# Kernel tuning notes

Hardware: AMD Instinct MI355X
Metric: run time of the kernel (lower is better)

The kernel has to match this reference:

```python
import jax, jax.numpy as jnp
import numpy as np


def gcn_conv(x, src, dst, W, b, n_nodes):
    # PyG GCNConv default: add self-loops, symmetric normalization D^-1/2 A D^-1/2.
    h = x @ W  # [N, out]
    # degree with unit edge weights + self loop
    deg = jnp.zeros((n_nodes,), dtype=x.dtype).at[dst].add(1.0) + 1.0
    dinv = jax.lax.rsqrt(deg)  # deg >= 1, safe
    norm = dinv[src] * dinv[dst]  # [E]
    msg = h[src] * norm[:, None]  # [E, out] gather + scale
    out = jnp.zeros_like(h).at[dst].add(msg)  # scatter-add aggregate
    # self-loop contribution: norm_ii = dinv_i^2
    out = out + h * (dinv * dinv)[:, None]
    return out + b


def setup_inputs() -> dict:
    key = jax.random.key(0)
    ks = jax.random.split(key, 10)
    N, E, F_in, H, G = 100000, 1600000, 128, 128, 256
    x = jax.random.normal(ks[0], (N, F_in), dtype=jnp.float32)
    edge_index = jax.random.randint(ks[1], (2, E), 0, N, dtype=jnp.int64)
    batch = jnp.sort(jax.random.randint(ks[2], (N,), 0, G, dtype=jnp.int64))
    s1 = 1.0 / np.sqrt(F_in)
    s2 = 1.0 / np.sqrt(H)
    W1 = jax.random.uniform(ks[3], (F_in, H), jnp.float32, -s1, s1)
    b1 = jnp.zeros((H,), jnp.float32)
    W2 = jax.random.uniform(ks[4], (H, H), jnp.float32, -s2, s2)
    b2 = jnp.zeros((H,), jnp.float32)
    Wlin = jax.random.uniform(ks[5], (H, 2), jnp.float32, -s2, s2)
    blin = jax.random.uniform(ks[6], (2,), jnp.float32, -s2, s2)
    return {"x": x, "edge_index": edge_index, "batch": batch, "num_graphs": G,
            "W1": W1, "b1": b1, "W2": W2, "b2": b2, "Wlin": Wlin, "blin": blin}


def reference(x, edge_index, batch, num_graphs, W1, b1, W2, b2, Wlin, blin):
    n_nodes = x.shape[0]
    src, dst = edge_index[0], edge_index[1]
    h = jax.nn.relu(gcn_conv(x, src, dst, W1, b1, n_nodes))
    h = jax.nn.relu(gcn_conv(h, src, dst, W2, b2, n_nodes))
    # global_mean_pool over graphs
    sums = jax.ops.segment_sum(h, batch, num_segments=num_graphs)
    counts = jax.ops.segment_sum(jnp.ones((n_nodes,), h.dtype), batch, num_segments=num_graphs)
    pooled = sums / jnp.maximum(counts, 1.0)[:, None]  # [G, H]
    return pooled @ Wlin + blin  # [G, 2]
```

## Files before the change

kernel.cpp:

```cpp
#include <hip/hip_runtime.h>
#include <hip/hip_bf16.h>


#define FEAT 128
#define GRAPHS 256
#define CH 2048
#define BSH 8
#define MAXNB 512

typedef short bf16x8 __attribute__((ext_vector_type(8)));
typedef float f32x4 __attribute__((ext_vector_type(4)));

__device__ inline unsigned bf16rne(float f) {
    unsigned u = __float_as_uint(f);
    return (u + 0x7FFFu + ((u >> 16) & 1u)) >> 16;
}
__device__ inline float bfl(unsigned u) { return __uint_as_float(u << 16); }
__device__ inline float bfh(unsigned u) { return __uint_as_float(u & 0xFFFF0000u); }

#define SWZ(row, kbyte) ((kbyte) ^ (((row) & 7) << 4))

__global__ __launch_bounds__(256) void k_setup(const float* __restrict__ W1,
                                               const float* __restrict__ W2,
                                               unsigned short* __restrict__ wpre1,
                                               unsigned short* __restrict__ wpre2,
                                               int* __restrict__ bhist, int NB) {
    int b = blockIdx.x;
    if (b < 16) {
        const float* W = (b < 8) ? W1 : W2;
        unsigned short* Wp = (b < 8) ? wpre1 : wpre2;
        int tid = (b & 7) * 256 + threadIdx.x;
        int frag = tid >> 6;
        int l = tid & 63;
        int cf = frag >> 2, ks = frag & 3;
        int col = cf * 16 + (l & 15);
        int k0 = ks * 32 + (l >> 4) * 8;
        unsigned short o[8];
#pragma unroll
        for (int j = 0; j < 8; ++j)
            o[j] = (unsigned short)bf16rne(W[(k0 + j) * 128 + col]);
        *(uint4*)(Wp + (size_t)tid * 8) = *(const uint4*)o;
    } else {
        for (int i = threadIdx.x; i < NB; i += 256) bhist[i] = 0;
    }
}

__global__ __launch_bounds__(256) void kb_hist(const int* __restrict__ dst, int E, int NB,
                                               int* __restrict__ bhist) {
    __shared__ int h[MAXNB];
    for (int i = threadIdx.x; i < NB; i += 256) h[i] = 0;
    __syncthreads();
    int stride = gridDim.x * 256;
    for (int i = blockIdx.x * 256 + threadIdx.x; i < E; i += stride)
        atomicAdd(&h[dst[i] >> BSH], 1);
    __syncthreads();
    for (int i = threadIdx.x; i < NB; i += 256)
        if (h[i]) atomicAdd(&bhist[i], h[i]);
}

__global__ void kb_scan(const int* __restrict__ bhist, int NB,
                        int* __restrict__ bbase, int* __restrict__ bcur) {
    __shared__ int s[512];
    int t = threadIdx.x;
    int v = (t < NB) ? bhist[t] : 0;
    s[t] = v;
    __syncthreads();
    for (int d = 1; d < 512; d <<= 1) {
        int a = (t >= d) ? s[t - d] : 0;
        __syncthreads();
        s[t] += a;
        __syncthreads();
    }
    if (t < NB) { int e = s[t] - v; bbase[t] = e; bcur[t] = e; }
}

__global__ __launch_bounds__(256) void kb_group(const int* __restrict__ src,
                                                const int* __restrict__ dst, int E, int NB,
                                                int* __restrict__ bcur,
                                                unsigned* __restrict__ stg) {
    __shared__ int lhist[MAXNB], lcur[MAXNB], gdelta[MAXNB], sc[512];
    __shared__ unsigned lpak[CH];
    __shared__ int gp[CH];
    int t = threadIdx.x;
    int base = blockIdx.x * CH;
    int n = E - base; if (n > CH) n = CH;

    for (int i = t; i < NB; i += 256) lhist[i] = 0;
    __syncthreads();

    unsigned pk[8]; int bk[8]; int nl = 0;
#pragma unroll
    for (int j = 0; j < 8; ++j) {
        int k = j * 256 + t;
        if (k < n) {
            int d = dst[base + k];
            int sv = src[base + k];
            int b = d >> BSH;
            pk[nl] = ((unsigned)(d & ((1 << BSH) - 1)) << 17) | (unsigned)sv;
            bk[nl] = b; nl++;
            atomicAdd(&lhist[b], 1);
        }
    }
    __syncthreads();

    for (int i = t; i < 512; i += 256) sc[i] = (i < NB) ? lhist[i] : 0;
    __syncthreads();
    for (int d = 1; d < 512; d <<= 1) {
        int a0 = (t >= d) ? sc[t - d] : 0;
        int a1 = sc[t + 256 - d];
        __syncthreads();
        sc[t] += a0; sc[t + 256] += a1;
        __syncthreads();
    }
    for (int i = t; i < NB; i += 256) {
        int c = lhist[i];
        int lb = sc[i] - c;
        lcur[i] = lb;
        int g = c ? atomicAdd(&bcur[i], c) : 0;
        gdelta[i] = g - lb;
    }
    __syncthreads();

    for (int j = 0; j < nl; ++j) {
        int b = bk[j];
        int slot = atomicAdd(&lcur[b], 1);
        lpak[slot] = pk[j];
        gp[slot] = gdelta[b] + slot;
    }
    __syncthreads();
    for (int i = t; i < n; i += 256) stg[gp[i]] = lpak[i];
}

__global__ __launch_bounds__(256) void kb_csr(const unsigned* __restrict__ stg,
                                              const int* __restrict__ bbase,
                                              const int* __restrict__ bhist, int N,
                                              int* __restrict__ ssrc, int* __restrict__ off,
                                              int* __restrict__ cnt, float* __restrict__ dinv) {
    __shared__ int h[256], lcur[256], sc[256];
    int b = blockIdx.x;
    int t = threadIdx.x;
    int s0 = bbase[b], m = bhist[b];
    h[t] = 0;
    __syncthreads();
    for (int i = t; i < m; i += 256) atomicAdd(&h[stg[s0 + i] >> 17], 1);
    __syncthreads();
    int v = h[t];
    sc[t] = v;
    __syncthreads();
    for (int d = 1; d < 256; d <<= 1) {
        int a = (t >= d) ? sc[t - d] : 0;
        __syncthreads();
        sc[t] += a;
        __syncthreads();
    }
    int lb = sc[t] - v;
    lcur[t] = lb;
    int node = (b << BSH) + t;
    if (node < N) {
        off[node] = s0 + lb;
        cnt[node] = v;
        dinv[node] = rsqrtf(1.0f + (float)v);
    }
    __syncthreads();
    for (int i = t; i < m; i += 256) {
        unsigned p = stg[s0 + i];
        int d = p >> 17;
        int r = atomicAdd(&lcur[d], 1);
        ssrc[s0 + r] = (int)(p & 0x1FFFFu);
    }
}

__global__ void k_gstart(const int* __restrict__ batch, int N, int G, int* __restrict__ gstart) {
    int i = blockIdx.x * blockDim.x + threadIdx.x;
    if (i >= N) return;
    int b = batch[i];
    int bp = (i == 0) ? -1 : batch[i - 1];
    for (int g = bp + 1; g <= b; ++g) gstart[g] = i;
    if (i == N - 1) {
        for (int g = b + 1; g <= G; ++g) gstart[g] = N;
    }
}

__device__ inline unsigned umax16pair(unsigned d, unsigned cur) {
    unsigned a = d & 0x7FFF7FFFu;
    unsigned lo = a & 0xFFFFu, hi = a >> 16;
    unsigned m = lo > hi ? lo : hi;
    return m > cur ? m : cur;
}
__device__ inline unsigned q8b(float x, float si) {
    return (unsigned)(__float2int_rn(x * si) + 128) & 0xFFu;
}
__device__ inline unsigned pack2(unsigned d0, unsigned d1, float si) {
    float x0 = bfl(d0), x1 = bfh(d0), x2 = bfl(d1), x3 = bfh(d1);
    return q8b(x0, si) | (q8b(x1, si) << 8) | (q8b(x2, si) << 16) | (q8b(x3, si) << 24);
}

template <bool BF16IN>
__global__ __launch_bounds__(256, 4) void k_gemm_mfma(const void* __restrict__ Xv,
                                                      const unsigned short* __restrict__ Wpre,
                                                      const float* __restrict__ dinv,
                                                      unsigned char* __restrict__ Q8,
                                                      float* __restrict__ srow, int N) {
    __shared__ __align__(16) unsigned short sA[128 * 128];
    __shared__ unsigned sMaxH[256];
    int t = threadIdx.x;
    int r0 = blockIdx.x * 128;
    int rows = N - r0; if (rows > 128) rows = 128;

    if constexpr (!BF16IN) {
        const float4* X4 = (const float4*)((const float*)Xv + (size_t)r0 * 128);
#pragma unroll
        for (int j = 0; j < 16; ++j) {
            int f = j * 256 + t;
            int row = f >> 5, q = f & 31;
            float4 v = make_float4(0.f, 0.f, 0.f, 0.f);
            if (row < rows) v = X4[f];
            unsigned lo = bf16rne(v.x) | (bf16rne(v.y) << 16);
            unsigned hi = bf16rne(v.z) | (bf16rne(v.w) << 16);
            int byte = row * 256 + SWZ(row, q * 8);
            *(uint2*)((char*)sA + byte) = make_uint2(lo, hi);
        }
    } else {
        const uint4* X4 = (const uint4*)((const unsigned short*)Xv + (size_t)r0 * 128);
#pragma unroll
        for (int j = 0; j < 8; ++j) {
            int f = j * 256 + t;
            int row = f >> 4, q = f & 15;
            uint4 v = make_uint4(0u, 0u, 0u, 0u);
            if (row < rows) v = X4[f];
            int byte = row * 256 + SWZ(row, q * 16);
            *(uint4*)((char*)sA + byte) = v;
        }
    }
    __syncthreads();

    int w = t >> 6, l = t & 63;
    int wr = (w >> 1) * 64, wc = (w & 1) * 64;
    int lr = l & 15, kc = l >> 4;

    f32x4 acc[4][4] = {};
    for (int ks = 0; ks < 4; ++ks) {
        bf16x8 a[4], b[4];
#pragma unroll
        for (int m = 0; m < 4; ++m) {
            int row = wr + m * 16 + lr;
            int byte = row * 256 + SWZ(row, ks * 64 + kc * 16);
            a[m] = *(const bf16x8*)((const char*)sA + byte);
        }
#pragma unroll
        for (int n = 0; n < 4; ++n) {
            int cf = (wc >> 4) + n;
            b[n] = *(const bf16x8*)(Wpre + ((size_t)((cf * 4 + ks) * 64 + l) * 8));
        }
#pragma unroll
        for (int m = 0; m < 4; ++m)
#pragma unroll
            for (int n = 0; n < 4; ++n)
                acc[m][n] = __builtin_amdgcn_mfma_f32_16x16x32_bf16(a[m], b[n], acc[m][n], 0, 0, 0);
    }
    __syncthreads();

#pragma unroll
    for (int m = 0; m < 4; ++m) {
        int rbase = wr + m * 16 + kc * 4;
#pragma unroll
        for (int r = 0; r < 4; ++r) {
            int row = rbase + r;
            float dv = (r0 + row < N) ? dinv[r0 + row] : 0.f;
#pragma unroll
            for (int n = 0; n < 4; ++n) {
                int col = wc + n * 16 + lr;
                sA[row * 128 + col] = (unsigned short)bf16rne(acc[m][n][r] * dv);
            }
        }
    }
    __syncthreads();

    {
        int r = t >> 1, hh = t & 1;
        const uint4* rowp = (const uint4*)(sA + r * 128 + hh * 64);
        uint4 wreg[8];
#pragma unroll
        for (int j = 0; j < 8; ++j) wreg[j] = rowp[j];
        unsigned mb = 0;
#pragma unroll
        for (int j = 0; j < 8; ++j) {
            mb = umax16pair(wreg[j].x, mb);
            mb = umax16pair(wreg[j].y, mb);
            mb = umax16pair(wreg[j].z, mb);
            mb = umax16pair(wreg[j].w, mb);
        }
        sMaxH[r * 2 + hh] = mb;
        __syncthreads();
        unsigned m0 = sMaxH[r * 2], m1 = sMaxH[r * 2 + 1];
        unsigned m16 = m0 > m1 ? m0 : m1;
        float mv = __uint_as_float(m16 << 16);
        float si = (mv > 0.f) ? 127.0f / mv : 0.0f;
        if (hh == 0 && r0 + r < N) srow[r0 + r] = mv * (1.0f / 127.0f);
        if (r0 + r < N) {
            unsigned q[16];
#pragma unroll
            for (int j = 0; j < 8; ++j) {
                q[2 * j]     = pack2(wreg[j].x, wreg[j].y, si);
                q[2 * j + 1] = pack2(wreg[j].z, wreg[j].w, si);
            }
            uint4* qo = (uint4*)(Q8 + (size_t)(r0 + r) * 128 + hh * 64);
            qo[0] = make_uint4(q[0], q[1], q[2], q[3]);
            qo[1] = make_uint4(q[4], q[5], q[6], q[7]);
            qo[2] = make_uint4(q[8], q[9], q[10], q[11]);
            qo[3] = make_uint4(q[12], q[13], q[14], q[15]);
        }
    }
}

#define ACCU(u, s, A, B, C, D) {                      \
    A = fmaf(s, (float)((u) & 0xFFu), A);             \
    B = fmaf(s, (float)(((u) >> 8) & 0xFFu), B);      \
    C = fmaf(s, (float)(((u) >> 16) & 0xFFu), C);     \
    D = fmaf(s, (float)((u) >> 24), D); }
#define ACCROW8(R, S) { float _s = (S); ssum += _s;   \
    ACCU(R.x, _s, a0, a1, a2, a3)                     \
    ACCU(R.y, _s, a4, a5, a6, a7)                     \
    ACCU(R.z, _s, a8, a9, a10, a11)                   \
    ACCU(R.w, _s, a12, a13, a14, a15) }

__global__ __launch_bounds__(256) void k_agg8(const unsigned char* __restrict__ Q8,
                                              const float* __restrict__ srow,
                                              const int* __restrict__ off,
                                              const int* __restrict__ cnt,
                                              const int* __restrict__ ssrc,
                                              const float* __restrict__ dinv,
                                              const float* __restrict__ b,
                                              unsigned* __restrict__ OUTB, int N) {
    int v = (blockIdx.x * blockDim.x + threadIdx.x) >> 3;
    if (v >= N) return;
    int j = threadIdx.x & 7;

    float a0 = 0.f, a1 = 0.f, a2 = 0.f, a3 = 0.f, a4 = 0.f, a5 = 0.f, a6 = 0.f, a7 = 0.f;
    float a8 = 0.f, a9 = 0.f, a10 = 0.f, a11 = 0.f, a12 = 0.f, a13 = 0.f, a14 = 0.f, a15 = 0.f;
    float ssum = 0.f;

    {
        uint4 r = *(const uint4*)(Q8 + (size_t)v * 128 + j * 16);
        float s = srow[v];
        ACCROW8(r, s)
    }
    int i = off[v], e = i + cnt[v];
    for (; i + 8 <= e; i += 8) {
        int4 ua = *(const int4*)(ssrc + i);
        int4 ub = *(const int4*)(ssrc + i + 4);
        uint4 r0 = *(const uint4*)(Q8 + (size_t)ua.x * 128 + j * 16);
        uint4 r1 = *(const uint4*)(Q8 + (size_t)ua.y * 128 + j * 16);
        uint4 r2 = *(const uint4*)(Q8 + (size_t)ua.z * 128 + j * 16);
        uint4 r3 = *(const uint4*)(Q8 + (size_t)ua.w * 128 + j * 16);
        uint4 r4 = *(const uint4*)(Q8 + (size_t)ub.x * 128 + j * 16);
        uint4 r5 = *(const uint4*)(Q8 + (size_t)ub.y * 128 + j * 16);
        uint4 r6 = *(const uint4*)(Q8 + (size_t)ub.z * 128 + j * 16);
        uint4 r7 = *(const uint4*)(Q8 + (size_t)ub.w * 128 + j * 16);
        float s0 = srow[ua.x], s1 = srow[ua.y], s2 = srow[ua.z], s3 = srow[ua.w];
        float s4 = srow[ub.x], s5 = srow[ub.y], s6 = srow[ub.z], s7 = srow[ub.w];
        ACCROW8(r0, s0) ACCROW8(r1, s1) ACCROW8(r2, s2) ACCROW8(r3, s3)
        ACCROW8(r4, s4) ACCROW8(r5, s5) ACCROW8(r6, s6) ACCROW8(r7, s7)
    }
    if (i + 4 <= e) {
        int4 ua = *(const int4*)(ssrc + i);
        uint4 r0 = *(const uint4*)(Q8 + (size_t)ua.x * 128 + j * 16);
        uint4 r1 = *(const uint4*)(Q8 + (size_t)ua.y * 128 + j * 16);
        uint4 r2 = *(const uint4*)(Q8 + (size_t)ua.z * 128 + j * 16);
        uint4 r3 = *(const uint4*)(Q8 + (size_t)ua.w * 128 + j * 16);
        float s0 = srow[ua.x], s1 = srow[ua.y], s2 = srow[ua.z], s3 = srow[ua.w];
        ACCROW8(r0, s0) ACCROW8(r1, s1) ACCROW8(r2, s2) ACCROW8(r3, s3)
        i += 4;
    }
    for (; i < e; ++i) {
        int u = ssrc[i];
        uint4 r = *(const uint4*)(Q8 + (size_t)u * 128 + j * 16);
        float s = srow[u];
        ACCROW8(r, s)
    }

    float dv = dinv[v];
    float corr = 128.f * ssum;
    const float4* B4 = (const float4*)(b + j * 16);
    float4 bb0 = B4[0], bb1 = B4[1], bb2 = B4[2], bb3 = B4[3];
    float o0  = fmaxf((a0  - corr) * dv + bb0.x, 0.f);
    float o1  = fmaxf((a1  - corr) * dv + bb0.y, 0.f);
    float o2  = fmaxf((a2  - corr) * dv + bb0.z, 0.f);
    float o3  = fmaxf((a3  - corr) * dv + bb0.w, 0.f);
    float o4  = fmaxf((a4  - corr) * dv + bb1.x, 0.f);
    float o5  = fmaxf((a5  - corr) * dv + bb1.y, 0.f);
    float o6  = fmaxf((a6  - corr) * dv + bb1.z, 0.f);
    float o7  = fmaxf((a7  - corr) * dv + bb1.w, 0.f);
    float o8  = fmaxf((a8  - corr) * dv + bb2.x, 0.f);
    float o9  = fmaxf((a9  - corr) * dv + bb2.y, 0.f);
    float o10 = fmaxf((a10 - corr) * dv + bb2.z, 0.f);
    float o11 = fmaxf((a11 - corr) * dv + bb2.w, 0.f);
    float o12 = fmaxf((a12 - corr) * dv + bb3.x, 0.f);
    float o13 = fmaxf((a13 - corr) * dv + bb3.y, 0.f);
    float o14 = fmaxf((a14 - corr) * dv + bb3.z, 0.f);
    float o15 = fmaxf((a15 - corr) * dv + bb3.w, 0.f);

    uint4 w0, w1;
    w0.x = bf16rne(o0)  | (bf16rne(o1)  << 16);
    w0.y = bf16rne(o2)  | (bf16rne(o3)  << 16);
    w0.z = bf16rne(o4)  | (bf16rne(o5)  << 16);
    w0.w = bf16rne(o6)  | (bf16rne(o7)  << 16);
    w1.x = bf16rne(o8)  | (bf16rne(o9)  << 16);
    w1.y = bf16rne(o10) | (bf16rne(o11) << 16);
    w1.z = bf16rne(o12) | (bf16rne(o13) << 16);
    w1.w = bf16rne(o14) | (bf16rne(o15) << 16);
    uint4* orow = (uint4*)OUTB + (size_t)v * 16 + j * 2;
    orow[0] = w0;
    orow[1] = w1;
}

__global__ __launch_bounds__(256) void k_pool_head(const unsigned* __restrict__ H2,
                                                   const int* __restrict__ gstart,
                                                   const float* __restrict__ Wlin,
                                                   const float* __restrict__ blin,
                                                   float* __restrict__ out, int G) {
    __shared__ float2 stmp[256];
    __shared__ float sp[128];
    int g = blockIdx.x;
    int t = threadIdx.x;
    int p = t & 63, quarter = t >> 6;
    int s = gstart[g], e = gstart[g + 1];
    float2 acc = make_float2(0.f, 0.f);
    for (int i = s + quarter; i < e; i += 4) {
        unsigned u = H2[(size_t)i * 64 + p];
        acc.x += bfl(u);
        acc.y += bfh(u);
    }
    stmp[t] = acc;
    __syncthreads();
    if (t < 64) {
        float2 a = stmp[t];
        a.x += stmp[t + 64].x + stmp[t + 128].x + stmp[t + 192].x;
        a.y += stmp[t + 64].y + stmp[t + 128].y + stmp[t + 192].y;
        float inv = 1.0f / fmaxf((float)(e - s), 1.0f);
        sp[2 * t] = a.x * inv;
        sp[2 * t + 1] = a.y * inv;
    }
    __syncthreads();
    if (t < 2) {
        float a = 0.0f;
        for (int j = 0; j < 128; ++j) a += sp[j] * Wlin[j * 2 + t];
        out[g * 2 + t] = a + blin[t];
    }
}

extern "C" void kernel_launch(void* const* d_in, const int* in_sizes, int n_in,
                              void* d_out, int out_size, void* d_ws, size_t ws_size,
                              hipStream_t stream) {
    const float* x     = (const float*)d_in[0];
    const int*   ei    = (const int*)d_in[1];
    const int*   batch = (const int*)d_in[2];
    const float* W1    = (const float*)d_in[4];
    const float* b1    = (const float*)d_in[5];
    const float* W2    = (const float*)d_in[6];
    const float* b2    = (const float*)d_in[7];
    const float* Wlin  = (const float*)d_in[8];
    const float* blin  = (const float*)d_in[9];
    float* out = (float*)d_out;

    const int N = in_sizes[0] / FEAT;
    const int E = in_sizes[1] / 2;
    const int G = GRAPHS;
    const int NB = (N + (1 << BSH) - 1) >> BSH;
    const int* src = ei;
    const int* dst = ei + E;

    char* ws = (char*)d_ws;
    unsigned char* q8 = (unsigned char*)ws;
    float* srow = (float*)(q8 + (size_t)N * FEAT);
    unsigned short* hact = (unsigned short*)(srow + N);
    int*   ssrc = (int*)(hact + (size_t)N * FEAT);
    unsigned* stg = (unsigned*)(ssrc + E);
    int*   off  = (int*)(stg + E);
    int*   cnt  = off + N;
    float* dinv = (float*)(cnt + N);
    int*   bhist = (int*)(dinv + N);
    int*   bbase = bhist + MAXNB;
    int*   bcur  = bbase + MAXNB;
    int*   gstart = bcur + MAXNB;
    unsigned short* wpre1 = (unsigned short*)(gstart + G + 2);
    unsigned short* wpre2 = wpre1 + 16384;

    const int nb = (N + 255) / 256;
    const int nch = (E + CH - 1) / CH;
    const int ngb = (N + 127) / 128;

    k_setup<<<17, 256, 0, stream>>>(W1, W2, wpre1, wpre2, bhist, NB);

    kb_hist<<<256, 256, 0, stream>>>(dst, E, NB, bhist);
    kb_scan<<<1, 512, 0, stream>>>(bhist, NB, bbase, bcur);
    kb_group<<<nch, 256, 0, stream>>>(src, dst, E, NB, bcur, stg);
    kb_csr<<<NB, 256, 0, stream>>>(stg, bbase, bhist, N, ssrc, off, cnt, dinv);

    k_gstart<<<nb, 256, 0, stream>>>(batch, N, G, gstart);

    k_gemm_mfma<false><<<ngb, 256, 0, stream>>>(x, wpre1, dinv, q8, srow, N);
    k_agg8<<<(N * 8 + 255) / 256, 256, 0, stream>>>(q8, srow, off, cnt, ssrc, dinv, b1, (unsigned*)hact, N);
    k_gemm_mfma<true><<<ngb, 256, 0, stream>>>(hact, wpre2, dinv, q8, srow, N);
    k_agg8<<<(N * 8 + 255) / 256, 256, 0, stream>>>(q8, srow, off, cnt, ssrc, dinv, b2, (unsigned*)hact, N);

    k_pool_head<<<G, 256, 0, stream>>>((const unsigned*)hact, gstart, Wlin, blin, out, G);
}
```

Baseline: 306.9 us.

## Sort nodes by degree within each bucket to balance aggregation wavefronts

The CSR build kernel now computes a per-256-node-bucket counting sort of nodes by in-degree (capped at 63) and writes a permutation array. The aggregation kernel maps each 8-thread group to perm[slot] instead of the raw node index, so nodes with similar degree share a wavefront and loop trip counts diverge less. The cost is an extra indirection load, an extra scan in kb_csr, and less contiguous output writes and self-row reads.

```diff
diff --git a/kernel.cpp b/kernel.cpp
--- a/kernel.cpp
+++ b/kernel.cpp
@@ -135,12 +135,15 @@
                                               const int* __restrict__ bbase,
                                               const int* __restrict__ bhist, int N,
                                               int* __restrict__ ssrc, int* __restrict__ off,
-                                              int* __restrict__ cnt, float* __restrict__ dinv) {
+                                              int* __restrict__ cnt, float* __restrict__ dinv,
+                                              int* __restrict__ perm) {
     __shared__ int h[256], lcur[256], sc[256];
+    __shared__ int dh[64], ds[64], dcur[64];
     int b = blockIdx.x;
     int t = threadIdx.x;
     int s0 = bbase[b], m = bhist[b];
     h[t] = 0;
+    if (t < 64) dh[t] = 0;
     __syncthreads();
     for (int i = t; i < m; i += 256) atomicAdd(&h[stg[s0 + i] >> 17], 1);
     __syncthreads();
@@ -156,10 +159,28 @@
     int lb = sc[t] - v;
     lcur[t] = lb;
     int node = (b << BSH) + t;
+    int cb = min(v, 63);
     if (node < N) {
         off[node] = s0 + lb;
         cnt[node] = v;
         dinv[node] = rsqrtf(1.0f + (float)v);
+        atomicAdd(&dh[cb], 1);
+    }
+    __syncthreads();
+    if (t < 64) ds[t] = dh[t];
+    __syncthreads();
+    for (int d = 1; d < 64; d <<= 1) {
+        int a = 0;
+        if (t < 64 && t >= d) a = ds[t - d];
+        __syncthreads();
+        if (t < 64) ds[t] += a;
+        __syncthreads();
+    }
+    if (t < 64) dcur[t] = ds[t] - dh[t];
+    __syncthreads();
+    if (node < N) {
+        int rank = atomicAdd(&dcur[cb], 1);
+        perm[(b << BSH) + rank] = node;
     }
     __syncthreads();
     for (int i = t; i < m; i += 256) {
@@ -329,12 +350,14 @@
                                               const int* __restrict__ off,
                                               const int* __restrict__ cnt,
                                               const int* __restrict__ ssrc,
+                                              const int* __restrict__ perm,
                                               const float* __restrict__ dinv,
                                               const float* __restrict__ b,
                                               unsigned* __restrict__ OUTB, int N) {
-    int v = (blockIdx.x * blockDim.x + threadIdx.x) >> 3;
-    if (v >= N) return;
+    int slot = (blockIdx.x * blockDim.x + threadIdx.x) >> 3;
+    if (slot >= N) return;
     int j = threadIdx.x & 7;
+    int v = perm[slot];
 
     float a0 = 0.f, a1 = 0.f, a2 = 0.f, a3 = 0.f, a4 = 0.f, a5 = 0.f, a6 = 0.f, a7 = 0.f;
     float a8 = 0.f, a9 = 0.f, a10 = 0.f, a11 = 0.f, a12 = 0.f, a13 = 0.f, a14 = 0.f, a15 = 0.f;
@@ -479,7 +502,8 @@
     int*   off  = (int*)(stg + E);
     int*   cnt  = off + N;
     float* dinv = (float*)(cnt + N);
-    int*   bhist = (int*)(dinv + N);
+    int*   perm = (int*)(dinv + N);
+    int*   bhist = perm + N;
     int*   bbase = bhist + MAXNB;
     int*   bcur  = bbase + MAXNB;
     int*   gstart = bcur + MAXNB;
@@ -495,14 +519,14 @@
     kb_hist<<<256, 256, 0, stream>>>(dst, E, NB, bhist);
     kb_scan<<<1, 512, 0, stream>>>(bhist, NB, bbase, bcur);
     kb_group<<<nch, 256, 0, stream>>>(src, dst, E, NB, bcur, stg);
-    kb_csr<<<NB, 256, 0, stream>>>(stg, bbase, bhist, N, ssrc, off, cnt, dinv);
+    kb_csr<<<NB, 256, 0, stream>>>(stg, bbase, bhist, N, ssrc, off, cnt, dinv, perm);
 
     k_gstart<<<nb, 256, 0, stream>>>(batch, N, G, gstart);
 
     k_gemm_mfma<false><<<ngb, 256, 0, stream>>>(x, wpre1, dinv, q8, srow, N);
-    k_agg8<<<(N * 8 + 255) / 256, 256, 0, stream>>>(q8, srow, off, cnt, ssrc, dinv, b1, (unsigned*)hact, N);
+    k_agg8<<<(N * 8 + 255) / 256, 256, 0, stream>>>(q8, srow, off, cnt, ssrc, perm, dinv, b1, (unsigned*)hact, N);
     k_gemm_mfma<true><<<ngb, 256, 0, stream>>>(hact, wpre2, dinv, q8, srow, N);
-    k_agg8<<<(N * 8 + 255) / 256, 256, 0, stream>>>(q8, srow, off, cnt, ssrc, dinv, b2, (unsigned*)hact, N);
+    k_agg8<<<(N * 8 + 255) / 256, 256, 0, stream>>>(q8, srow, off, cnt, ssrc, perm, dinv, b2, (unsigned*)hact, N);
 
     k_pool_head<<<G, 256, 0, stream>>>((const unsigned*)hact, gstart, Wlin, blin, out, G);
 }
```

Result: slower. 322.3 us (+5.0%).
